# Kernel tuning notes

Measured on AMD Instinct MI355X. Metric: run time of the kernel, lower is better.

Reference implementation:

```python
import jax, jax.numpy as jnp
import numpy as np

B, H, W, N, C = 2, 56, 56, 2, 128
NUM_HEADS = 8
SPLIT = 7
IDX = 0  # 0 -> H_sp = H, W_sp = split_size (vertical stripes)


def setup_inputs() -> dict:
    key = jax.random.key(0)
    k1, k2, k3, k4 = jax.random.split(key, 4)
    query = jax.random.normal(k1, (B, H, W, N, C), jnp.float32)
    key_t = jax.random.normal(k2, (B, H, W, N, C), jnp.float32)
    value = jax.random.normal(k3, (B, H, W, N, C), jnp.float32)
    conv_w = jax.random.normal(k4, (C, 1, 3, 3), jnp.float32) * 0.1  # depthwise get_v weight
    return {"query": query, "key": key_t, "value": value, "conv_w": conv_w}


def _im2cswin(x, Hsp, Wsp, h):
    # [b, Hp, Wp, n, c] -> [(b i j), h, Hsp*Wsp*n, d]
    b, Hp, Wp, n, c = x.shape
    i, j = Hp // Hsp, Wp // Wsp
    d = c // h
    x = x.reshape(b, i, Hsp, j, Wsp, n, h, d)
    x = x.transpose(0, 1, 3, 6, 2, 4, 5, 7)  # b i j h Hsp Wsp n d
    return x.reshape(b * i * j, h, Hsp * Wsp * n, d)


def _window_mask(Hsp, Wsp, n):
    # block attention between same spatial position / different candidates (except diagonal)
    pos = jnp.repeat(jnp.arange(Hsp * Wsp), n)
    L = pos.shape[0]
    m = jnp.where(pos[:, None] == pos[None, :], -jnp.inf, 0.0).astype(jnp.float32)
    m = m.at[jnp.arange(L), jnp.arange(L)].set(0.0)
    return m


def reference(query, key, value, conv_w):
    b, Hh, Ww, n, c = query.shape
    if IDX == -1:
        Hsp, Wsp = Hh, Ww
    elif IDX == 0:
        Hsp, Wsp = Hh, SPLIT
    else:
        Hsp, Wsp = SPLIT, Ww
    # H % Hsp == 0 and W % Wsp == 0 by construction -> no padding branch
    h = NUM_HEADS
    d = c // h
    scale = d ** (-0.5)

    q = _im2cswin(query, Hsp, Wsp, h)
    k = _im2cswin(key, Hsp, Wsp, h)
    v = _im2cswin(value, Hsp, Wsp, h)

    # rpe via depthwise 3x3 conv over the value (LePE-style), summed over candidates
    v_img = value.transpose(0, 3, 4, 1, 2).reshape(b * n, c, Hh, Ww)  # [b*n, C, H, W]
    conv = jax.lax.conv_general_dilated(
        v_img, conv_w, (1, 1), 'SAME',
        dimension_numbers=('NCHW', 'OIHW', 'NCHW'), feature_group_count=c)
    rpe = conv.reshape(b, n, c, Hh, Ww).sum(1, keepdims=True)
    center = conv_w[:, 0, 1, 1]  # center tap of each depthwise kernel
    self_scaled = (v_img * center[None, :, None, None]).reshape(b, n, c, Hh, Ww)
    self_scaled = self_scaled - self_scaled.sum(1, keepdims=True)
    rpe = (rpe + self_scaled).transpose(0, 3, 4, 1, 2)  # [b, H, W, n, c]

    mask = _window_mask(Hsp, Wsp, n)[None, None]  # [1,1,L,L]
    attn = jnp.einsum('bhid,bhjd->bhij', q * scale, k) + mask
    attn = jax.nn.softmax(attn.astype(jnp.float32), axis=-1).astype(q.dtype)
    x = jnp.einsum('bhij,bhjd->bhid', attn, v)

    # windows back to image layout
    i, j = Hh // Hsp, Ww // Wsp
    x = x.reshape(b, i, j, h, Hsp, Wsp, n, d)
    x = x.transpose(0, 1, 4, 2, 5, 6, 3, 7).reshape(b, Hh, Ww, n, c)
    return x + rpe
```

## Files before the change

### kernel.cpp

```cpp
#include <hip/hip_runtime.h>

typedef __bf16 bf16x8 __attribute__((ext_vector_type(8)));
typedef float f32x16 __attribute__((ext_vector_type(16)));
typedef unsigned u32x2 __attribute__((ext_vector_type(2)));

#define BB 2
#define HH 56
#define WW 56
#define NN 2
#define CC 128
#define NH 8
#define DD 16
#define WSP 7
#define LQ 784
#define KB_TOK 800
#define VT_STRIDE 808
#define NQT 25
#define NKC 25
#define NINST 128
#define NW 4
#define VT_OFF 12800
#define SLICE_ELEMS 26536
#define YSTRIP 7
#define NB_RPE 448
#define NB_PACK 404
#define YSTRD 14336
#define BSTRD 802816

#define QSCALE 0.3606737602222409f

union U2 { __bf16 h[2]; unsigned u; };
union U4 { unsigned u[4]; bf16x8 v; };
union H8 { bf16x8 v; uint4 q; };

__global__ __launch_bounds__(256) void prep_kernel(const float* __restrict__ value,
                                                   const float* __restrict__ conv_w,
                                                   const float* __restrict__ k_g,
                                                   float* __restrict__ out,
                                                   __bf16* __restrict__ ws) {
    const int bx = blockIdx.x;
    const int tid = threadIdx.x;

    if (bx < NB_RPE) {
        const int b     = bx / 224;
        const int r0    = bx - b * 224;
        const int strip = r0 / 28;
        const int blk   = r0 - strip * 28;
        const int idx   = blk * 256 + tid;
        const int c     = idx & 127;
        const int x     = idx >> 7;
        const int y0    = strip * YSTRIP;

        float w[9];
#pragma unroll
        for (int k = 0; k < 9; ++k) w[k] = conv_w[c * 9 + k];
        const float center = w[4];

        const float* vb = value + (long)b * BSTRD + x * (NN * CC) + c;
        float* ob = out + (long)b * BSTRD + x * (NN * CC) + c;
        const bool xm = x > 0, xp = x < WW - 1;

        auto loadS = [&](int y, int dx) -> float {
            const float* p = vb + y * YSTRD + dx * (NN * CC);
            return p[0] + p[CC];
        };

        float sm[3], s0[3], sp[3];
        if (y0 > 0) {
            sm[0] = xm ? loadS(y0 - 1, -1) : 0.f;
            sm[1] = loadS(y0 - 1, 0);
            sm[2] = xp ? loadS(y0 - 1, 1) : 0.f;
        } else { sm[0] = sm[1] = sm[2] = 0.f; }
        s0[0] = xm ? loadS(y0, -1) : 0.f;
        s0[1] = loadS(y0, 0);
        s0[2] = xp ? loadS(y0, 1) : 0.f;

#pragma unroll
        for (int yy = 0; yy < YSTRIP; ++yy) {
            const int y = y0 + yy;
            if (y + 1 < HH) {
                sp[0] = xm ? loadS(y + 1, -1) : 0.f;
                sp[1] = loadS(y + 1, 0);
                sp[2] = xp ? loadS(y + 1, 1) : 0.f;
            } else { sp[0] = sp[1] = sp[2] = 0.f; }

            float conv_sum = w[0] * sm[0] + w[1] * sm[1] + w[2] * sm[2]
                           + w[3] * s0[0] + w[4] * s0[1] + w[5] * s0[2]
                           + w[6] * sp[0] + w[7] * sp[1] + w[8] * sp[2];
            float v0 = vb[y * YSTRD];
            float v1 = s0[1] - v0;
            float base = conv_sum - center * s0[1];
            float* po = ob + y * YSTRD;
            po[0]  = base + center * v0;
            po[CC] = base + center * v1;

            sm[0] = s0[0]; sm[1] = s0[1]; sm[2] = s0[2];
            s0[0] = sp[0]; s0[1] = sp[1]; s0[2] = sp[2];
        }
    } else {
        int idx = (bx - NB_RPE) * 256 + tid;
        int inst = idx / VT_STRIDE;
        int tok  = idx - inst * VT_STRIDE;

        __bf16* kbase = ws + (long)inst * SLICE_ELEMS;
        __bf16* vbase = kbase + VT_OFF;

        vbase[16 * VT_STRIDE + tok] = (__bf16)1.f;

        if (tok >= LQ) {
            if (tok < KB_TOK) {
                H8 z; z.q = make_uint4(0, 0, 0, 0);
                uint4* kq = (uint4*)(kbase + tok * 16);
                kq[0] = z.q; kq[1] = z.q;
            }
#pragma unroll
            for (int d = 0; d < 16; ++d)
                vbase[d * VT_STRIDE + tok] = (__bf16)0.f;
            return;
        }

        int head = inst & 7, win = inst >> 3;
        int b = win >> 3, wj = win & 7;
        int pos = tok >> 1, n = tok & 1;
        int y = pos / WSP, xl = pos - y * WSP;
        long off = ((long)(((b * HH + y) * WW + wj * WSP + xl) * NN + n)) * CC + head * DD;

        float kv[16], vv[16];
        *(float4*)&kv[0]  = *(const float4*)(k_g + off);
        *(float4*)&kv[4]  = *(const float4*)(k_g + off + 4);
        *(float4*)&kv[8]  = *(const float4*)(k_g + off + 8);
        *(float4*)&kv[12] = *(const float4*)(k_g + off + 12);
        *(float4*)&vv[0]  = *(const float4*)(value + off);
        *(float4*)&vv[4]  = *(const float4*)(value + off + 4);
        *(float4*)&vv[8]  = *(const float4*)(value + off + 8);
        *(float4*)&vv[12] = *(const float4*)(value + off + 12);

        H8 lo, hi;
#pragma unroll
        for (int i = 0; i < 8; ++i) { lo.v[i] = (__bf16)kv[i]; hi.v[i] = (__bf16)kv[8 + i]; }
        uint4* kq = (uint4*)(kbase + tok * 16);
        kq[0] = lo.q;
        kq[1] = hi.q;

#pragma unroll
        for (int d = 0; d < 16; ++d)
            vbase[d * VT_STRIDE + tok] = (__bf16)vv[d];
    }
}

__global__ __launch_bounds__(256) void attn_mfma(const float* __restrict__ q_g,
                                                 const __bf16* __restrict__ ws,
                                                 float* __restrict__ out) {
    __shared__ float red[NW][64][11];

    const int bid  = blockIdx.x;
    const int slot = bid >> 3;
    const int inst = (bid & 7) + 8 * (slot / 25);
    const int qt   = slot % 25;
    const int head = inst & 7;
    const int win  = inst >> 3;

    const int tid  = threadIdx.x;
    const int w    = tid >> 6;
    const int lane = tid & 63;
    const int col  = lane & 31;
    const int h    = lane >> 5;
    const int q0   = qt * 32;
    const int myq  = q0 + col;
    const int sib  = myq ^ 1;

    const int myqc = myq < LQ ? myq : LQ - 1;
    const int b = win >> 3, wj = win & 7;
    const int pos = myqc >> 1, n = myqc & 1;
    const int y = pos / WSP, xl = pos - y * WSP;
    const long ooff = ((long)(((b * HH + y) * WW + wj * WSP + xl) * NN + n)) * CC + head * DD;

    bf16x8 qfv;
    {
        const float* qp = q_g + ooff + 8 * h;
        float qv[8];
        *(float4*)&qv[0] = *(const float4*)qp;
        *(float4*)&qv[4] = *(const float4*)(qp + 4);
        H8 qq;
#pragma unroll
        for (int i = 0; i < 8; ++i) qq.v[i] = (__bf16)(qv[i] * QSCALE);
        qfv = qq.v;
    }

    f32x16 acc, zv;
#pragma unroll
    for (int i = 0; i < 16; ++i) { acc[i] = 0.f; zv[i] = 0.f; }

    const __bf16* base = ws + (long)inst * SLICE_ELEMS;
    const bf16x8* kpb = (const bf16x8*)base + col * 2 + h;
    const int vrow = col < 16 ? col : 16;
    const __bf16* vp = base + VT_OFF + vrow * VT_STRIDE + 8 * h;

    for (int c = w; c < NKC; c += NW) {
        bf16x8 kf = kpb[(long)c * 64];

        f32x16 st = __builtin_amdgcn_mfma_f32_32x32x16_bf16(kf, qfv, zv, 0, 0, 0);

        float p[16];
        if (c == qt || c == NKC - 1) {
#pragma unroll
            for (int r = 0; r < 16; ++r) {
                int kr = (r & 3) + 8 * (r >> 2) + 4 * h;
                int gk = c * 32 + kr;
                p[r] = (gk >= LQ || gk == sib) ? 0.f : __builtin_amdgcn_exp2f(st[r]);
            }
        } else {
#pragma unroll
            for (int r = 0; r < 16; ++r) p[r] = __builtin_amdgcn_exp2f(st[r]);
        }

        unsigned pk[4][2];
#pragma unroll
        for (int b2 = 0; b2 < 4; ++b2) {
            U2 a, bb;
            a.h[0]  = (__bf16)p[4 * b2 + 0];
            a.h[1]  = (__bf16)p[4 * b2 + 1];
            bb.h[0] = (__bf16)p[4 * b2 + 2];
            bb.h[1] = (__bf16)p[4 * b2 + 3];
            pk[b2][0] = a.u;
            pk[b2][1] = bb.u;
        }

#pragma unroll
        for (int t = 0; t < 2; ++t) {
            U4 pb;
#pragma unroll
            for (int j = 0; j < 2; ++j) {
#if __has_builtin(__builtin_amdgcn_permlane32_swap)
                u32x2 rr = __builtin_amdgcn_permlane32_swap(pk[2 * t][j], pk[2 * t + 1][j], false, false);
                pb.u[j]     = rr[0];
                pb.u[2 + j] = rr[1];
#else
                unsigned swa = __shfl_xor(pk[2 * t][j], 32, 64);
                unsigned swb = __shfl_xor(pk[2 * t + 1][j], 32, 64);
                pb.u[j]     = h ? swb : pk[2 * t][j];
                pb.u[2 + j] = h ? pk[2 * t + 1][j] : swa;
#endif
            }
            bf16x8 vf = *(const bf16x8*)(vp + c * 32 + 16 * t);
            acc = __builtin_amdgcn_mfma_f32_32x32x16_bf16(vf, pb.v, acc, 0, 0, 0);
        }
    }

#pragma unroll
    for (int i = 0; i < 9; ++i) red[w][lane][i] = acc[i];
    __syncthreads();

    if (w == 0 && myq < LQ) {
        float o[9];
#pragma unroll
        for (int i = 0; i < 9; ++i)
            o[i] = (red[0][lane][i] + red[1][lane][i]) + (red[2][lane][i] + red[3][lane][i]);
        float inv = 1.f / o[8];
        float* po = out + ooff;
        float4 r0 = *(float4*)(po + 4 * h);
        r0.x += o[0] * inv; r0.y += o[1] * inv;
        r0.z += o[2] * inv; r0.w += o[3] * inv;
        *(float4*)(po + 4 * h) = r0;
        float4 r1 = *(float4*)(po + 8 + 4 * h);
        r1.x += o[4] * inv; r1.y += o[5] * inv;
        r1.z += o[6] * inv; r1.w += o[7] * inv;
        *(float4*)(po + 8 + 4 * h) = r1;
    }
}

extern "C" void kernel_launch(void* const* d_in, const int* in_sizes, int n_in,
                              void* d_out, int out_size, void* d_ws, size_t ws_size,
                              hipStream_t stream) {
    const float* q = (const float*)d_in[0];
    const float* k = (const float*)d_in[1];
    const float* v = (const float*)d_in[2];
    const float* w = (const float*)d_in[3];
    float* out = (float*)d_out;

    __bf16* ws = (__bf16*)d_ws;

    prep_kernel<<<NB_RPE + NB_PACK, 256, 0, stream>>>(v, w, k, out, ws);

    attn_mfma<<<NQT * NH * 16, 256, 0, stream>>>(q, ws, out);
}
```

Before: 44.89 us.

## Fuse K/V packing into attention kernel via LDS staging, drop split-K reduction

The separate pack stage that wrote bf16 K and transposed V to a global workspace is removed. Each attention block now loads its instance's K/V from global fp32, converts them and stages them in shared memory. Each wave then processes a full query tile over all key chunks instead of splitting keys across waves, which eliminates the LDS cross-wave reduction. In exchange, each instance's K/V is loaded and converted redundantly by 5 blocks, per-wave serial work grows from about 7 to 25 key chunks, and the larger LDS footprint may reduce occupancy.

```diff
diff --git a/kernel.cpp b/kernel.cpp
--- a/kernel.cpp
+++ b/kernel.cpp
@@ -15,15 +15,12 @@
 #define LQ 784
 #define KB_TOK 800
 #define VT_STRIDE 808
-#define NQT 25
 #define NKC 25
 #define NINST 128
-#define NW 4
-#define VT_OFF 12800
-#define SLICE_ELEMS 26536
+#define BPI 5
+#define NWAVE 5
 #define YSTRIP 7
 #define NB_RPE 448
-#define NB_PACK 404
 #define YSTRD 14336
 #define BSTRD 802816
 
@@ -33,144 +30,130 @@
 union U4 { unsigned u[4]; bf16x8 v; };
 union H8 { bf16x8 v; uint4 q; };
 
-__global__ __launch_bounds__(256) void prep_kernel(const float* __restrict__ value,
-                                                   const float* __restrict__ conv_w,
-                                                   const float* __restrict__ k_g,
-                                                   float* __restrict__ out,
-                                                   __bf16* __restrict__ ws) {
+__global__ __launch_bounds__(256) void rpe_kernel(const float* __restrict__ value,
+                                                  const float* __restrict__ conv_w,
+                                                  float* __restrict__ out) {
     const int bx = blockIdx.x;
     const int tid = threadIdx.x;
-
-    if (bx < NB_RPE) {
-        const int b     = bx / 224;
-        const int r0    = bx - b * 224;
-        const int strip = r0 / 28;
-        const int blk   = r0 - strip * 28;
-        const int idx   = blk * 256 + tid;
-        const int c     = idx & 127;
-        const int x     = idx >> 7;
-        const int y0    = strip * YSTRIP;
-
-        float w[9];
-#pragma unroll
-        for (int k = 0; k < 9; ++k) w[k] = conv_w[c * 9 + k];
-        const float center = w[4];
-
-        const float* vb = value + (long)b * BSTRD + x * (NN * CC) + c;
-        float* ob = out + (long)b * BSTRD + x * (NN * CC) + c;
-        const bool xm = x > 0, xp = x < WW - 1;
-
-        auto loadS = [&](int y, int dx) -> float {
-            const float* p = vb + y * YSTRD + dx * (NN * CC);
-            return p[0] + p[CC];
-        };
-
-        float sm[3], s0[3], sp[3];
-        if (y0 > 0) {
-            sm[0] = xm ? loadS(y0 - 1, -1) : 0.f;
-            sm[1] = loadS(y0 - 1, 0);
-            sm[2] = xp ? loadS(y0 - 1, 1) : 0.f;
-        } else { sm[0] = sm[1] = sm[2] = 0.f; }
-        s0[0] = xm ? loadS(y0, -1) : 0.f;
-        s0[1] = loadS(y0, 0);
-        s0[2] = xp ? loadS(y0, 1) : 0.f;
-
-#pragma unroll
-        for (int yy = 0; yy < YSTRIP; ++yy) {
-            const int y = y0 + yy;
-            if (y + 1 < HH) {
-                sp[0] = xm ? loadS(y + 1, -1) : 0.f;
-                sp[1] = loadS(y + 1, 0);
-                sp[2] = xp ? loadS(y + 1, 1) : 0.f;
-            } else { sp[0] = sp[1] = sp[2] = 0.f; }
-
-            float conv_sum = w[0] * sm[0] + w[1] * sm[1] + w[2] * sm[2]
-                           + w[3] * s0[0] + w[4] * s0[1] + w[5] * s0[2]
-                           + w[6] * sp[0] + w[7] * sp[1] + w[8] * sp[2];
-            float v0 = vb[y * YSTRD];
-            float v1 = s0[1] - v0;
-            float base = conv_sum - center * s0[1];
-            float* po = ob + y * YSTRD;
-            po[0]  = base + center * v0;
-            po[CC] = base + center * v1;
-
-            sm[0] = s0[0]; sm[1] = s0[1]; sm[2] = s0[2];
-            s0[0] = sp[0]; s0[1] = sp[1]; s0[2] = sp[2];
-        }
-    } else {
-        int idx = (bx - NB_RPE) * 256 + tid;
-        int inst = idx / VT_STRIDE;
-        int tok  = idx - inst * VT_STRIDE;
-
-        __bf16* kbase = ws + (long)inst * SLICE_ELEMS;
-        __bf16* vbase = kbase + VT_OFF;
-
-        vbase[16 * VT_STRIDE + tok] = (__bf16)1.f;
-
-        if (tok >= LQ) {
-            if (tok < KB_TOK) {
-                H8 z; z.q = make_uint4(0, 0, 0, 0);
-                uint4* kq = (uint4*)(kbase + tok * 16);
-                kq[0] = z.q; kq[1] = z.q;
-            }
-#pragma unroll
-            for (int d = 0; d < 16; ++d)
-                vbase[d * VT_STRIDE + tok] = (__bf16)0.f;
-            return;
-        }
-
-        int head = inst & 7, win = inst >> 3;
-        int b = win >> 3, wj = win & 7;
-        int pos = tok >> 1, n = tok & 1;
-        int y = pos / WSP, xl = pos - y * WSP;
-        long off = ((long)(((b * HH + y) * WW + wj * WSP + xl) * NN + n)) * CC + head * DD;
-
-        float kv[16], vv[16];
-        *(float4*)&kv[0]  = *(const float4*)(k_g + off);
-        *(float4*)&kv[4]  = *(const float4*)(k_g + off + 4);
-        *(float4*)&kv[8]  = *(const float4*)(k_g + off + 8);
-        *(float4*)&kv[12] = *(const float4*)(k_g + off + 12);
-        *(float4*)&vv[0]  = *(const float4*)(value + off);
-        *(float4*)&vv[4]  = *(const float4*)(value + off + 4);
-        *(float4*)&vv[8]  = *(const float4*)(value + off + 8);
-        *(float4*)&vv[12] = *(const float4*)(value + off + 12);
-
-        H8 lo, hi;
-#pragma unroll
-        for (int i = 0; i < 8; ++i) { lo.v[i] = (__bf16)kv[i]; hi.v[i] = (__bf16)kv[8 + i]; }
-        uint4* kq = (uint4*)(kbase + tok * 16);
-        kq[0] = lo.q;
-        kq[1] = hi.q;
-
-#pragma unroll
-        for (int d = 0; d < 16; ++d)
-            vbase[d * VT_STRIDE + tok] = (__bf16)vv[d];
+    const int b     = bx / 224;
+    const int r0    = bx - b * 224;
+    const int strip = r0 / 28;
+    const int blk   = r0 - strip * 28;
+    const int idx   = blk * 256 + tid;
+    const int c     = idx & 127;
+    const int x     = idx >> 7;
+    const int y0    = strip * YSTRIP;
+
+    float w[9];
+#pragma unroll
+    for (int k = 0; k < 9; ++k) w[k] = conv_w[c * 9 + k];
+    const float center = w[4];
+
+    const float* vb = value + (long)b * BSTRD + x * (NN * CC) + c;
+    float* ob = out + (long)b * BSTRD + x * (NN * CC) + c;
+    const bool xm = x > 0, xp = x < WW - 1;
+
+    auto loadS = [&](int y, int dx) -> float {
+        const float* p = vb + y * YSTRD + dx * (NN * CC);
+        return p[0] + p[CC];
+    };
+
+    float sm[3], s0[3], sp[3];
+    if (y0 > 0) {
+        sm[0] = xm ? loadS(y0 - 1, -1) : 0.f;
+        sm[1] = loadS(y0 - 1, 0);
+        sm[2] = xp ? loadS(y0 - 1, 1) : 0.f;
+    } else { sm[0] = sm[1] = sm[2] = 0.f; }
+    s0[0] = xm ? loadS(y0, -1) : 0.f;
+    s0[1] = loadS(y0, 0);
+    s0[2] = xp ? loadS(y0, 1) : 0.f;
+
+#pragma unroll
+    for (int yy = 0; yy < YSTRIP; ++yy) {
+        const int y = y0 + yy;
+        if (y + 1 < HH) {
+            sp[0] = xm ? loadS(y + 1, -1) : 0.f;
+            sp[1] = loadS(y + 1, 0);
+            sp[2] = xp ? loadS(y + 1, 1) : 0.f;
+        } else { sp[0] = sp[1] = sp[2] = 0.f; }
+
+        float conv_sum = w[0] * sm[0] + w[1] * sm[1] + w[2] * sm[2]
+                       + w[3] * s0[0] + w[4] * s0[1] + w[5] * s0[2]
+                       + w[6] * sp[0] + w[7] * sp[1] + w[8] * sp[2];
+        float v0 = vb[y * YSTRD];
+        float v1 = s0[1] - v0;
+        float base = conv_sum - center * s0[1];
+        float* po = ob + y * YSTRD;
+        po[0]  = base + center * v0;
+        po[CC] = base + center * v1;
+
+        sm[0] = s0[0]; sm[1] = s0[1]; sm[2] = s0[2];
+        s0[0] = sp[0]; s0[1] = sp[1]; s0[2] = sp[2];
     }
 }
 
-__global__ __launch_bounds__(256) void attn_mfma(const float* __restrict__ q_g,
-                                                 const __bf16* __restrict__ ws,
-                                                 float* __restrict__ out) {
-    __shared__ float red[NW][64][11];
+__global__ __launch_bounds__(320) void attn_fused(const float* __restrict__ q_g,
+                                                  const float* __restrict__ k_g,
+                                                  const float* __restrict__ v_g,
+                                                  float* __restrict__ out) {
+    __shared__ alignas(16) __bf16 Klds[KB_TOK * 16];
+    __shared__ alignas(16) __bf16 Vlds[17 * VT_STRIDE];
 
     const int bid  = blockIdx.x;
-    const int slot = bid >> 3;
-    const int inst = (bid & 7) + 8 * (slot / 25);
-    const int qt   = slot % 25;
+    const int g    = bid >> 3;
+    const int inst = (bid & 7) + 8 * (g / BPI);
+    const int part = g % BPI;
     const int head = inst & 7;
     const int win  = inst >> 3;
+    const int b    = win >> 3, wj = win & 7;
 
     const int tid  = threadIdx.x;
+
+    for (int tok = tid; tok < KB_TOK; tok += 320) {
+        Vlds[16 * VT_STRIDE + tok] = (__bf16)1.f;
+        if (tok < LQ) {
+            int pos = tok >> 1, n = tok & 1;
+            int y = pos / WSP, xl = pos - y * WSP;
+            long off = ((long)(((b * HH + y) * WW + wj * WSP + xl) * NN + n)) * CC + head * DD;
+
+            float kv[16], vv[16];
+            *(float4*)&kv[0]  = *(const float4*)(k_g + off);
+            *(float4*)&kv[4]  = *(const float4*)(k_g + off + 4);
+            *(float4*)&kv[8]  = *(const float4*)(k_g + off + 8);
+            *(float4*)&kv[12] = *(const float4*)(k_g + off + 12);
+            *(float4*)&vv[0]  = *(const float4*)(v_g + off);
+            *(float4*)&vv[4]  = *(const float4*)(v_g + off + 4);
+            *(float4*)&vv[8]  = *(const float4*)(v_g + off + 8);
+            *(float4*)&vv[12] = *(const float4*)(v_g + off + 12);
+
+            H8 lo, hi;
+#pragma unroll
+            for (int i = 0; i < 8; ++i) { lo.v[i] = (__bf16)kv[i]; hi.v[i] = (__bf16)kv[8 + i]; }
+            *(uint4*)&Klds[tok * 16]     = lo.q;
+            *(uint4*)&Klds[tok * 16 + 8] = hi.q;
+#pragma unroll
+            for (int d = 0; d < 16; ++d)
+                Vlds[d * VT_STRIDE + tok] = (__bf16)vv[d];
+        } else {
+            H8 z; z.q = make_uint4(0, 0, 0, 0);
+            *(uint4*)&Klds[tok * 16]     = z.q;
+            *(uint4*)&Klds[tok * 16 + 8] = z.q;
+#pragma unroll
+            for (int d = 0; d < 16; ++d)
+                Vlds[d * VT_STRIDE + tok] = (__bf16)0.f;
+        }
+    }
+    __syncthreads();
+
     const int w    = tid >> 6;
     const int lane = tid & 63;
     const int col  = lane & 31;
     const int h    = lane >> 5;
-    const int q0   = qt * 32;
-    const int myq  = q0 + col;
+    const int qt   = part * NWAVE + w;
+    const int myq  = qt * 32 + col;
     const int sib  = myq ^ 1;
 
     const int myqc = myq < LQ ? myq : LQ - 1;
-    const int b = win >> 3, wj = win & 7;
     const int pos = myqc >> 1, n = myqc & 1;
     const int y = pos / WSP, xl = pos - y * WSP;
     const long ooff = ((long)(((b * HH + y) * WW + wj * WSP + xl) * NN + n)) * CC + head * DD;
@@ -191,13 +174,12 @@
 #pragma unroll
     for (int i = 0; i < 16; ++i) { acc[i] = 0.f; zv[i] = 0.f; }
 
-    const __bf16* base = ws + (long)inst * SLICE_ELEMS;
-    const bf16x8* kpb = (const bf16x8*)base + col * 2 + h;
+    const char* kbase = (const char*)Klds + col * 32 + h * 16;
     const int vrow = col < 16 ? col : 16;
-    const __bf16* vp = base + VT_OFF + vrow * VT_STRIDE + 8 * h;
-
-    for (int c = w; c < NKC; c += NW) {
-        bf16x8 kf = kpb[(long)c * 64];
+    const char* vbase = (const char*)Vlds + vrow * (VT_STRIDE * 2) + h * 16;
+
+    for (int c = 0; c < NKC; ++c) {
+        bf16x8 kf = *(const bf16x8*)(kbase + c * 1024);
 
         f32x16 st = __builtin_amdgcn_mfma_f32_32x32x16_bf16(kf, qfv, zv, 0, 0, 0);
 
@@ -242,29 +224,21 @@
                 pb.u[2 + j] = h ? pk[2 * t + 1][j] : swa;
 #endif
             }
-            bf16x8 vf = *(const bf16x8*)(vp + c * 32 + 16 * t);
+            bf16x8 vf = *(const bf16x8*)(vbase + c * 64 + t * 32);
             acc = __builtin_amdgcn_mfma_f32_32x32x16_bf16(vf, pb.v, acc, 0, 0, 0);
         }
     }
 
-#pragma unroll
-    for (int i = 0; i < 9; ++i) red[w][lane][i] = acc[i];
-    __syncthreads();
-
-    if (w == 0 && myq < LQ) {
-        float o[9];
-#pragma unroll
-        for (int i = 0; i < 9; ++i)
-            o[i] = (red[0][lane][i] + red[1][lane][i]) + (red[2][lane][i] + red[3][lane][i]);
-        float inv = 1.f / o[8];
+    if (myq < LQ) {
+        float inv = 1.f / acc[8];
         float* po = out + ooff;
         float4 r0 = *(float4*)(po + 4 * h);
-        r0.x += o[0] * inv; r0.y += o[1] * inv;
-        r0.z += o[2] * inv; r0.w += o[3] * inv;
+        r0.x += acc[0] * inv; r0.y += acc[1] * inv;
+        r0.z += acc[2] * inv; r0.w += acc[3] * inv;
         *(float4*)(po + 4 * h) = r0;
         float4 r1 = *(float4*)(po + 8 + 4 * h);
-        r1.x += o[4] * inv; r1.y += o[5] * inv;
-        r1.z += o[6] * inv; r1.w += o[7] * inv;
+        r1.x += acc[4] * inv; r1.y += acc[5] * inv;
+        r1.z += acc[6] * inv; r1.w += acc[7] * inv;
         *(float4*)(po + 8 + 4 * h) = r1;
     }
 }
@@ -278,9 +252,7 @@
     const float* w = (const float*)d_in[3];
     float* out = (float*)d_out;
 
-    __bf16* ws = (__bf16*)d_ws;
-
-    prep_kernel<<<NB_RPE + NB_PACK, 256, 0, stream>>>(v, w, k, out, ws);
-
-    attn_mfma<<<NQT * NH * 16, 256, 0, stream>>>(q, ws, out);
+    rpe_kernel<<<NB_RPE, 256, 0, stream>>>(v, w, out);
+
+    attn_fused<<<NINST * BPI, 320, 0, stream>>>(q, k, v, out);
 }
```

New measurement: 44.81 us. No clear change (-0.2%).
